# Optimization experiments

Measured on AMD Instinct MI355X. Metric: run time of the kernel, lower is better.

Reference implementation:

```python
import jax, jax.numpy as jnp
import numpy as np

N = 200000   # nodes
E = 600000   # directed edges
G = 8192     # graphs in batch
D_IN = 30
H = 128


def setup_inputs() -> dict:
    key = jax.random.key(0)
    ks = jax.random.split(key, 9)
    x = jax.random.normal(ks[0], (N, D_IN), jnp.float32)
    edge_index = jax.random.randint(ks[1], (2, E), 0, N, dtype=jnp.int32)
    batch_idx = jnp.sort(jax.random.randint(ks[2], (N,), 0, G, dtype=jnp.int32))
    W1 = jax.random.normal(ks[3], (D_IN, H), jnp.float32) / np.sqrt(D_IN)
    b1 = jnp.zeros((H,), jnp.float32)
    W2 = jax.random.normal(ks[4], (H, H), jnp.float32) / np.sqrt(H)
    b2 = jnp.zeros((H,), jnp.float32)
    W3 = jax.random.normal(ks[5], (H, H), jnp.float32) / np.sqrt(H)
    b3 = jnp.zeros((H,), jnp.float32)
    return {"x": x, "edge_index": edge_index, "batch_idx": batch_idx,
            "W1": W1, "b1": b1, "W2": W2, "b2": b2, "W3": W3, "b3": b3}


def _gcn_layer(x, W, b, src, dst, dinv):
    h = x @ W                                   # [N, H]
    norm = (dinv[src] * dinv[dst])[:, None]     # per-edge normalization
    msg = h[src] * norm                         # [E, H] gather + scale
    agg = jax.ops.segment_sum(msg, dst, num_segments=N)
    agg = agg + h * (dinv * dinv)[:, None]      # self-loop term, norm = 1/deg
    return jax.nn.relu(agg + b)


def reference(x, edge_index, batch_idx, W1, b1, W2, b2, W3, b3):
    src, dst = edge_index[0], edge_index[1]
    # degree with self-loops (edge weight 1), aggregated at target (col)
    deg = 1.0 + jax.ops.segment_sum(jnp.ones((E,), x.dtype), dst, num_segments=N)
    dinv = jax.lax.rsqrt(deg)                   # deg >= 1, safe
    h = _gcn_layer(x, W1, b1, src, dst, dinv)
    h = _gcn_layer(h, W2, b2, src, dst, dinv)
    h = _gcn_layer(h, W3, b3, src, dst, dinv)
    # global mean pool over batch segments
    sums = jax.ops.segment_sum(h, batch_idx, num_segments=G)
    counts = jax.ops.segment_sum(jnp.ones((N,), h.dtype), batch_idx, num_segments=G)
    return sums / jnp.maximum(counts, 1.0)[:, None]
```

## Files before the change

### kernel.cpp

```cpp
#include <hip/hip_runtime.h>


#define DIN 30
#define HD  128

typedef __attribute__((ext_vector_type(8))) short v8s;
typedef __attribute__((ext_vector_type(4))) float v4f;

static __device__ __forceinline__ unsigned short f2bf(float f) {
  unsigned int u = __float_as_uint(f);
  u += 0x7fffu + ((u >> 16) & 1u);
  return (unsigned short)(u >> 16);
}
static __device__ __forceinline__ float bf2f(unsigned short s) {
  return __uint_as_float(((unsigned int)s) << 16);
}
static __device__ __forceinline__ float bflo(unsigned int u) {
  return __uint_as_float(u << 16);
}
static __device__ __forceinline__ float bfhi(unsigned int u) {
  return __uint_as_float(u & 0xffff0000u);
}

__global__ void k_degree(const int* __restrict__ dst, int* __restrict__ deg,
                         int* __restrict__ eord, int E) {
  int e = blockIdx.x * blockDim.x + threadIdx.x;
  if (e < E) eord[e] = atomicAdd(&deg[dst[e]], 1);
}

__global__ void k_scan(const int* __restrict__ deg, int* __restrict__ scanbuf,
                       int* __restrict__ rowptr, float* __restrict__ dinv, int N) {
  __shared__ int s[256];
  __shared__ int sbase;
  int bid = blockIdx.x, tid = threadIdx.x;
  int base = bid * 1024 + tid * 4;
  int v[4]; int t = 0;
#pragma unroll
  for (int j = 0; j < 4; ++j) { int idx = base + j; v[j] = (idx < N) ? deg[idx] : 0; t += v[j]; }
  s[tid] = t; __syncthreads();
  for (int d = 1; d < 256; d <<= 1) {
    int u = (tid >= d) ? s[tid - d] : 0;
    __syncthreads();
    s[tid] += u;
    __syncthreads();
  }
  int myexcl = s[tid] - t;
  int blocktotal = s[255];
  if (tid == 0) atomicExch(&scanbuf[bid], blocktotal | 0x80000000);

  int pre = 0;
  for (int p = tid; p < bid; p += 256) {
    int val;
    do { val = atomicAdd(&scanbuf[p], 0); } while (!(val & 0x80000000));
    pre += val & 0x7fffffff;
  }
  __syncthreads();
  s[tid] = pre; __syncthreads();
  for (int d = 128; d > 0; d >>= 1) { if (tid < d) s[tid] += s[tid + d]; __syncthreads(); }
  if (tid == 0) sbase = s[0];
  __syncthreads();

  int run = sbase + myexcl;
#pragma unroll
  for (int j = 0; j < 4; ++j) {
    int idx = base + j;
    if (idx < N) {
      rowptr[idx] = run;
      dinv[idx] = rsqrtf((float)(1 + v[j]));
    }
    run += v[j];
    if (idx == N - 1) rowptr[N] = run;
  }
}

static __device__ __forceinline__ void wtf_one(const float* __restrict__ W,
                                               unsigned short* __restrict__ WTF,
                                               int idx, int Kreal, int KK) {
  int j = idx & 7;
  int c = idx >> 3;
  int l15 = c & 15;
  int quad = (c >> 4) & 3;
  int kk = (c >> 6) % KK;
  int t = c / (64 * KK);
  int k = kk * 32 + quad * 8 + j;
  int n = t * 16 + l15;
  WTF[idx] = (k < Kreal) ? f2bf(W[k * 128 + n]) : (unsigned short)0;
}

__global__ void k_prep(const int* __restrict__ src, const int* __restrict__ dst,
                       const int* __restrict__ rowptr, const int* __restrict__ eord,
                       int* __restrict__ col, int E,
                       const float* __restrict__ x, const float* __restrict__ dinv,
                       unsigned short* __restrict__ xb, int N,
                       const float* __restrict__ W1, const float* __restrict__ W2,
                       const float* __restrict__ W3,
                       unsigned short* __restrict__ W1F, unsigned short* __restrict__ W2F,
                       unsigned short* __restrict__ W3F,
                       const int* __restrict__ batch, int* __restrict__ gstart, int G,
                       float* __restrict__ out,
                       int SB, int XB, int WB, int BB) {
  int blk = blockIdx.x;
  if (blk < SB) {
    int e = blk * 256 + threadIdx.x;
    if (e < E) col[rowptr[dst[e]] + eord[e]] = src[e];
  } else if (blk < SB + XB) {
    int idx = (blk - SB) * 256 + threadIdx.x;
    if (idx < N * 32) {
      int n = idx >> 5, f = idx & 31;
      float v = (f < DIN) ? x[(size_t)n * DIN + f] * dinv[n] : 0.f;
      xb[idx] = f2bf(v);
    }
  } else if (blk < SB + XB + WB) {
    int idx = (blk - SB - XB) * 256 + threadIdx.x;
    if (idx < 4096) wtf_one(W1, W1F, idx, DIN, 1);
    else if (idx < 20480) wtf_one(W2, W2F, idx - 4096, 128, 4);
    else if (idx < 36864) wtf_one(W3, W3F, idx - 20480, 128, 4);
  } else if (blk < SB + XB + WB + BB) {
    int i = (blk - SB - XB - WB) * 256 + threadIdx.x;
    if (i >= N) return;
    int b = batch[i];
    int prev = (i == 0) ? -1 : batch[i - 1];
    for (int g = prev + 1; g <= b; ++g) gstart[g] = i;
    if (i == N - 1)
      for (int g = b + 1; g <= G; ++g) gstart[g] = N;
  } else {
    int idx = (blk - SB - XB - WB - BB) * 256 + threadIdx.x;
    if (idx < G * 32)
      ((float4*)out)[idx] = make_float4(0.f, 0.f, 0.f, 0.f);
  }
}

template <int K>
__global__ __launch_bounds__(1024, 8) void k_fused(const unsigned short* __restrict__ hin,
                                                   const unsigned short* __restrict__ WTF,
                                                   const float* __restrict__ b,
                                                   const int* __restrict__ rowptr,
                                                   const int* __restrict__ col,
                                                   const float* __restrict__ dinv,
                                                   unsigned short* __restrict__ C, int N) {
  constexpr int KK = K / 32;
  constexpr int KP = (K == 128) ? 136 : 40;
  constexpr int CP = 132;
  constexpr int SMSZ = (64 * KP > 64 * CP) ? 64 * KP : 64 * CP;
  __shared__ __align__(16) unsigned short sm[SMSZ];

  int tid = threadIdx.x;
  int l16 = tid & 15;
  int nl = tid >> 4;
  int row0 = blockIdx.x * 64;
  int node = row0 + nl;

  if (K == 32) {
    const unsigned int* hp = (const unsigned int*)hin;
    float a0 = 0.f, a1 = 0.f;
    if (node < N) {
      unsigned int u = hp[(size_t)node * 16 + l16];
      a0 = bflo(u); a1 = bfhi(u);
      int e0 = rowptr[node], e1 = rowptr[node + 1];
      int e = e0;
      for (; e + 2 <= e1; e += 2) {
        int c0 = col[e], c1 = col[e + 1];
        unsigned int v0 = hp[(size_t)c0 * 16 + l16];
        unsigned int v1 = hp[(size_t)c1 * 16 + l16];
        a0 += bflo(v0); a1 += bfhi(v0);
        a0 += bflo(v1); a1 += bfhi(v1);
      }
      if (e < e1) {
        unsigned int v0 = hp[(size_t)col[e] * 16 + l16];
        a0 += bflo(v0); a1 += bfhi(v0);
      }
      float di = dinv[node];
      a0 *= di; a1 *= di;
    }
    *(unsigned int*)&sm[nl * KP + l16 * 2] =
        (unsigned int)f2bf(a0) | ((unsigned int)f2bf(a1) << 16);
  } else {
    const uint4* hp = (const uint4*)hin;
    float a0 = 0.f, a1 = 0.f, a2 = 0.f, a3 = 0.f, a4 = 0.f, a5 = 0.f, a6 = 0.f, a7 = 0.f;
    if (node < N) {
      uint4 u = hp[(size_t)node * 16 + l16];
      a0 = bflo(u.x); a1 = bfhi(u.x);
      a2 = bflo(u.y); a3 = bfhi(u.y);
      a4 = bflo(u.z); a5 = bfhi(u.z);
      a6 = bflo(u.w); a7 = bfhi(u.w);
      int e0 = rowptr[node], e1 = rowptr[node + 1];
      int e = e0;
      for (; e + 2 <= e1; e += 2) {
        int c0 = col[e], c1 = col[e + 1];
        uint4 v0 = hp[(size_t)c0 * 16 + l16];
        uint4 v1 = hp[(size_t)c1 * 16 + l16];
        a0 += bflo(v0.x); a1 += bfhi(v0.x);
        a2 += bflo(v0.y); a3 += bfhi(v0.y);
        a4 += bflo(v0.z); a5 += bfhi(v0.z);
        a6 += bflo(v0.w); a7 += bfhi(v0.w);
        a0 += bflo(v1.x); a1 += bfhi(v1.x);
        a2 += bflo(v1.y); a3 += bfhi(v1.y);
        a4 += bflo(v1.z); a5 += bfhi(v1.z);
        a6 += bflo(v1.w); a7 += bfhi(v1.w);
      }
      if (e < e1) {
        uint4 v0 = hp[(size_t)col[e] * 16 + l16];
        a0 += bflo(v0.x); a1 += bfhi(v0.x);
        a2 += bflo(v0.y); a3 += bfhi(v0.y);
        a4 += bflo(v0.z); a5 += bfhi(v0.z);
        a6 += bflo(v0.w); a7 += bfhi(v0.w);
      }
      float di = dinv[node];
      a0 *= di; a1 *= di; a2 *= di; a3 *= di;
      a4 *= di; a5 *= di; a6 *= di; a7 *= di;
    }
    uint4 o;
    o.x = (unsigned int)f2bf(a0) | ((unsigned int)f2bf(a1) << 16);
    o.y = (unsigned int)f2bf(a2) | ((unsigned int)f2bf(a3) << 16);
    o.z = (unsigned int)f2bf(a4) | ((unsigned int)f2bf(a5) << 16);
    o.w = (unsigned int)f2bf(a6) | ((unsigned int)f2bf(a7) << 16);
    *(uint4*)&sm[nl * KP + l16 * 8] = o;
  }
  __syncthreads();

  int wv = tid >> 6, lane = tid & 63, quad = lane >> 4, l15 = lane & 15;
  int rt = wv & 3, tp = wv >> 2;
  v8s af[KK];
#pragma unroll
  for (int kk = 0; kk < KK; ++kk)
    af[kk] = *(const v8s*)&sm[(rt * 16 + l15) * KP + kk * 32 + quad * 8];
  __syncthreads();

  int crow0 = row0 + rt * 16 + quad * 4;
  float dr[4];
  if (crow0 + 3 < N) {
    float4 d4 = *(const float4*)&dinv[crow0];
    dr[0] = d4.x; dr[1] = d4.y; dr[2] = d4.z; dr[3] = d4.w;
  } else {
#pragma unroll
    for (int i = 0; i < 4; ++i) dr[i] = (crow0 + i < N) ? dinv[crow0 + i] : 0.f;
  }

#pragma unroll
  for (int tt = 0; tt < 2; ++tt) {
    int t = tp * 2 + tt;
    v4f acc = {0.f, 0.f, 0.f, 0.f};
#pragma unroll
    for (int kk = 0; kk < KK; ++kk) {
      v8s bf = *(const v8s*)(WTF + (size_t)(((t * KK + kk) * 4 + quad) * 16 + l15) * 8);
      acc = __builtin_amdgcn_mfma_f32_16x16x32_bf16(af[kk], bf, acc, 0, 0, 0);
    }
    float bias = b[t * 16 + l15];
#pragma unroll
    for (int i = 0; i < 4; ++i) {
      float o = fmaxf(acc[i] + bias, 0.f) * dr[i];
      sm[(rt * 16 + quad * 4 + i) * CP + t * 16 + l15] = f2bf(o);
    }
  }
  __syncthreads();

#pragma unroll
  for (int j = 0; j < 2; ++j) {
    int linear = j * 1024 + tid;
    int r = linear >> 5, ch = linear & 31;
    uint2 v = *(const uint2*)&sm[r * CP + ch * 4];
    int row = row0 + r;
    if (row < N) ((uint2*)C)[(size_t)row * 32 + ch] = v;
  }
}

__global__ __launch_bounds__(1024, 8) void k_fused_pool(const unsigned short* __restrict__ hin,
                                                        const unsigned short* __restrict__ WTF,
                                                        const float* __restrict__ b,
                                                        const int* __restrict__ rowptr,
                                                        const int* __restrict__ col,
                                                        const float* __restrict__ dinv,
                                                        const int* __restrict__ batch,
                                                        float* __restrict__ out, int N) {
  constexpr int KK = 4, KP = 136, CP = 132;
  constexpr int SMSZ = 64 * KP;
  __shared__ __align__(16) unsigned short sm[SMSZ];
  __shared__ int sbatch[64];

  int tid = threadIdx.x;
  int l16 = tid & 15;
  int nl = tid >> 4;
  int row0 = blockIdx.x * 64;
  int node = row0 + nl;

  if (tid < 64) sbatch[tid] = (row0 + tid < N) ? batch[row0 + tid] : -1;

  {
    const uint4* hp = (const uint4*)hin;
    float a0 = 0.f, a1 = 0.f, a2 = 0.f, a3 = 0.f, a4 = 0.f, a5 = 0.f, a6 = 0.f, a7 = 0.f;
    if (node < N) {
      uint4 u = hp[(size_t)node * 16 + l16];
      a0 = bflo(u.x); a1 = bfhi(u.x);
      a2 = bflo(u.y); a3 = bfhi(u.y);
      a4 = bflo(u.z); a5 = bfhi(u.z);
      a6 = bflo(u.w); a7 = bfhi(u.w);
      int e0 = rowptr[node], e1 = rowptr[node + 1];
      int e = e0;
      for (; e + 2 <= e1; e += 2) {
        int c0 = col[e], c1 = col[e + 1];
        uint4 v0 = hp[(size_t)c0 * 16 + l16];
        uint4 v1 = hp[(size_t)c1 * 16 + l16];
        a0 += bflo(v0.x); a1 += bfhi(v0.x);
        a2 += bflo(v0.y); a3 += bfhi(v0.y);
        a4 += bflo(v0.z); a5 += bfhi(v0.z);
        a6 += bflo(v0.w); a7 += bfhi(v0.w);
        a0 += bflo(v1.x); a1 += bfhi(v1.x);
        a2 += bflo(v1.y); a3 += bfhi(v1.y);
        a4 += bflo(v1.z); a5 += bfhi(v1.z);
        a6 += bflo(v1.w); a7 += bfhi(v1.w);
      }
      if (e < e1) {
        uint4 v0 = hp[(size_t)col[e] * 16 + l16];
        a0 += bflo(v0.x); a1 += bfhi(v0.x);
        a2 += bflo(v0.y); a3 += bfhi(v0.y);
        a4 += bflo(v0.z); a5 += bfhi(v0.z);
        a6 += bflo(v0.w); a7 += bfhi(v0.w);
      }
      float di = dinv[node];
      a0 *= di; a1 *= di; a2 *= di; a3 *= di;
      a4 *= di; a5 *= di; a6 *= di; a7 *= di;
    }
    uint4 o;
    o.x = (unsigned int)f2bf(a0) | ((unsigned int)f2bf(a1) << 16);
    o.y = (unsigned int)f2bf(a2) | ((unsigned int)f2bf(a3) << 16);
    o.z = (unsigned int)f2bf(a4) | ((unsigned int)f2bf(a5) << 16);
    o.w = (unsigned int)f2bf(a6) | ((unsigned int)f2bf(a7) << 16);
    *(uint4*)&sm[nl * KP + l16 * 8] = o;
  }
  __syncthreads();

  int wv = tid >> 6, lane = tid & 63, quad = lane >> 4, l15 = lane & 15;
  int rt = wv & 3, tp = wv >> 2;
  v8s af[KK];
#pragma unroll
  for (int kk = 0; kk < KK; ++kk)
    af[kk] = *(const v8s*)&sm[(rt * 16 + l15) * KP + kk * 32 + quad * 8];
  __syncthreads();

#pragma unroll
  for (int tt = 0; tt < 2; ++tt) {
    int t = tp * 2 + tt;
    v4f acc = {0.f, 0.f, 0.f, 0.f};
#pragma unroll
    for (int kk = 0; kk < KK; ++kk) {
      v8s bf = *(const v8s*)(WTF + (size_t)(((t * KK + kk) * 4 + quad) * 16 + l15) * 8);
      acc = __builtin_amdgcn_mfma_f32_16x16x32_bf16(af[kk], bf, acc, 0, 0, 0);
    }
    float bias = b[t * 16 + l15];
#pragma unroll
    for (int i = 0; i < 4; ++i) {
      float o = fmaxf(acc[i] + bias, 0.f);
      sm[(rt * 16 + quad * 4 + i) * CP + t * 16 + l15] = f2bf(o);
    }
  }
  __syncthreads();

  int f = tid & 127;
  int grp = tid >> 7;
  float run = 0.f;
  int cur = -1;
#pragma unroll
  for (int j = 0; j < 8; ++j) {
    int r = grp * 8 + j;
    int g = sbatch[r];
    if (g != cur) {
      if (cur >= 0) atomicAdd(&out[(size_t)cur * 128 + f], run);
      run = 0.f; cur = g;
    }
    if (g >= 0) run += bf2f(sm[r * CP + f]);
  }
  if (cur >= 0) atomicAdd(&out[(size_t)cur * 128 + f], run);
}

__global__ void k_finalize(float* __restrict__ out, const int* __restrict__ gstart, int G) {
  int idx = blockIdx.x * blockDim.x + threadIdx.x;
  if (idx >= G * 128) return;
  int g = idx >> 7;
  float cnt = (float)(gstart[g + 1] - gstart[g]);
  out[idx] = out[idx] / fmaxf(cnt, 1.f);
}

extern "C" void kernel_launch(void* const* d_in, const int* in_sizes, int n_in,
                              void* d_out, int out_size, void* d_ws, size_t ws_size,
                              hipStream_t stream) {
  const float* x  = (const float*)d_in[0];
  const int* ei   = (const int*)d_in[1];
  const int* batch = (const int*)d_in[2];
  const float* W1 = (const float*)d_in[3];
  const float* b1 = (const float*)d_in[4];
  const float* W2 = (const float*)d_in[5];
  const float* b2 = (const float*)d_in[6];
  const float* W3 = (const float*)d_in[7];
  const float* b3 = (const float*)d_in[8];
  float* out = (float*)d_out;
  int N = in_sizes[2];
  int E = in_sizes[1] / 2;
  int G = out_size / HD;
  const int* src = ei;
  const int* dst = ei + E;

  size_t off = 0;
  char* ws = (char*)d_ws;
  auto alloc = [&](size_t bytes) -> void* {
    void* p = ws + off;
    off += (bytes + 255) & ~(size_t)255;
    return p;
  };
  int nb1024 = (N + 1023) / 1024;
  int*   deg     = (int*)alloc((size_t)N * 4);
  int*   scanbuf = (int*)alloc((size_t)nb1024 * 4);
  float* dinv    = (float*)alloc((size_t)N * 4);
  int*   rowptr  = (int*)alloc((size_t)(N + 1) * 4);
  int*   eord    = (int*)alloc((size_t)E * 4);
  int*   col     = (int*)alloc((size_t)E * 4);
  int*   gstart  = (int*)alloc((size_t)(G + 1) * 4);
  unsigned short* xb  = (unsigned short*)alloc((size_t)N * 32 * 2);
  unsigned short* hA  = (unsigned short*)alloc((size_t)N * HD * 2);
  unsigned short* hB  = (unsigned short*)alloc((size_t)N * HD * 2);
  unsigned short* W1F = (unsigned short*)alloc(4096 * 2);
  unsigned short* W2F = (unsigned short*)alloc(16384 * 2);
  unsigned short* W3F = (unsigned short*)alloc(16384 * 2);
  (void)ws_size; (void)n_in;

  size_t zbytes = (size_t)((char*)dinv - (char*)deg);
  hipMemsetAsync(deg, 0, zbytes, stream);
  k_degree<<<(E + 255) / 256, 256, 0, stream>>>(dst, deg, eord, E);
  k_scan<<<nb1024, 256, 0, stream>>>(deg, scanbuf, rowptr, dinv, N);

  int SB = (E + 255) / 256;
  int XB = (N * 32 + 255) / 256;
  int WB = 144;
  int BB = (N + 255) / 256;
  int ZB = (G * 32 + 255) / 256;
  k_prep<<<SB + XB + WB + BB + ZB, 256, 0, stream>>>(src, dst, rowptr, eord, col, E,
                                                     x, dinv, xb, N,
                                                     W1, W2, W3, W1F, W2F, W3F,
                                                     batch, gstart, G, out,
                                                     SB, XB, WB, BB);

  int fusedBlocks = (N + 63) / 64;
  k_fused<32><<<fusedBlocks, 1024, 0, stream>>>(xb, W1F, b1, rowptr, col, dinv, hA, N);
  k_fused<128><<<fusedBlocks, 1024, 0, stream>>>(hA, W2F, b2, rowptr, col, dinv, hB, N);
  k_fused_pool<<<fusedBlocks, 1024, 0, stream>>>(hB, W3F, b3, rowptr, col, dinv, batch, out, N);
  k_finalize<<<(G * 128 + 255) / 256, 256, 0, stream>>>(out, gstart, G);
}
```

Measured before the change: 295.3 us.

## Sort CSR neighbor lists and sweep gathers in source-index windows for cache locality

Adds a kernel that insertion-sorts each node's neighbor column list, then restructures the gather loops in all three fused layers to walk source indices in windows, with a block-wide barrier between windows. All threads in a block then gather from the same region of the feature table at roughly the same time, which is meant to improve L2 hit rates on random gathers. In exchange it adds the sort kernel, roughly N/WDW barriers per block (about 13 for the 128-wide layers and 4 for the first layer), a dependent col load inside the loop, and loses the two-way unrolled loads.

```diff
diff --git a/kernel.cpp b/kernel.cpp
--- a/kernel.cpp
+++ b/kernel.cpp
@@ -130,6 +130,18 @@
   }
 }
 
+__global__ void k_sortrows(const int* __restrict__ rowptr, int* __restrict__ col, int N) {
+  int n = blockIdx.x * blockDim.x + threadIdx.x;
+  if (n >= N) return;
+  int e0 = rowptr[n], e1 = rowptr[n + 1];
+  for (int i = e0 + 1; i < e1; ++i) {
+    int v = col[i];
+    int j = i - 1;
+    while (j >= e0 && col[j] > v) { col[j + 1] = col[j]; --j; }
+    col[j + 1] = v;
+  }
+}
+
 template <int K>
 __global__ __launch_bounds__(1024, 8) void k_fused(const unsigned short* __restrict__ hin,
                                                    const unsigned short* __restrict__ WTF,
@@ -142,6 +154,7 @@
   constexpr int KP = (K == 128) ? 136 : 40;
   constexpr int CP = 132;
   constexpr int SMSZ = (64 * KP > 64 * CP) ? 64 * KP : 64 * CP;
+  constexpr int WDW = (K == 32) ? 65536 : 16384;
   __shared__ __align__(16) unsigned short sm[SMSZ];
 
   int tid = threadIdx.x;
@@ -153,22 +166,24 @@
   if (K == 32) {
     const unsigned int* hp = (const unsigned int*)hin;
     float a0 = 0.f, a1 = 0.f;
+    int e = 0, e1 = 0;
     if (node < N) {
       unsigned int u = hp[(size_t)node * 16 + l16];
       a0 = bflo(u); a1 = bfhi(u);
-      int e0 = rowptr[node], e1 = rowptr[node + 1];
-      int e = e0;
-      for (; e + 2 <= e1; e += 2) {
-        int c0 = col[e], c1 = col[e + 1];
-        unsigned int v0 = hp[(size_t)c0 * 16 + l16];
-        unsigned int v1 = hp[(size_t)c1 * 16 + l16];
-        a0 += bflo(v0); a1 += bfhi(v0);
-        a0 += bflo(v1); a1 += bfhi(v1);
-      }
-      if (e < e1) {
-        unsigned int v0 = hp[(size_t)col[e] * 16 + l16];
+      e = rowptr[node]; e1 = rowptr[node + 1];
+    }
+    int nc = (e < e1) ? col[e] : 0x7fffffff;
+    for (int lim = WDW;; lim += WDW) {
+      while (nc < lim) {
+        unsigned int v0 = hp[(size_t)nc * 16 + l16];
+        ++e;
+        nc = (e < e1) ? col[e] : 0x7fffffff;
         a0 += bflo(v0); a1 += bfhi(v0);
       }
+      if (lim >= N) break;
+      __syncthreads();
+    }
+    if (node < N) {
       float di = dinv[node];
       a0 *= di; a1 *= di;
     }
@@ -177,34 +192,30 @@
   } else {
     const uint4* hp = (const uint4*)hin;
     float a0 = 0.f, a1 = 0.f, a2 = 0.f, a3 = 0.f, a4 = 0.f, a5 = 0.f, a6 = 0.f, a7 = 0.f;
+    int e = 0, e1 = 0;
     if (node < N) {
       uint4 u = hp[(size_t)node * 16 + l16];
       a0 = bflo(u.x); a1 = bfhi(u.x);
       a2 = bflo(u.y); a3 = bfhi(u.y);
       a4 = bflo(u.z); a5 = bfhi(u.z);
       a6 = bflo(u.w); a7 = bfhi(u.w);
-      int e0 = rowptr[node], e1 = rowptr[node + 1];
-      int e = e0;
-      for (; e + 2 <= e1; e += 2) {
-        int c0 = col[e], c1 = col[e + 1];
-        uint4 v0 = hp[(size_t)c0 * 16 + l16];
-        uint4 v1 = hp[(size_t)c1 * 16 + l16];
-        a0 += bflo(v0.x); a1 += bfhi(v0.x);
-        a2 += bflo(v0.y); a3 += bfhi(v0.y);
-        a4 += bflo(v0.z); a5 += bfhi(v0.z);
-        a6 += bflo(v0.w); a7 += bfhi(v0.w);
-        a0 += bflo(v1.x); a1 += bfhi(v1.x);
-        a2 += bflo(v1.y); a3 += bfhi(v1.y);
-        a4 += bflo(v1.z); a5 += bfhi(v1.z);
-        a6 += bflo(v1.w); a7 += bfhi(v1.w);
-      }
-      if (e < e1) {
-        uint4 v0 = hp[(size_t)col[e] * 16 + l16];
+      e = rowptr[node]; e1 = rowptr[node + 1];
+    }
+    int nc = (e < e1) ? col[e] : 0x7fffffff;
+    for (int lim = WDW;; lim += WDW) {
+      while (nc < lim) {
+        uint4 v0 = hp[(size_t)nc * 16 + l16];
+        ++e;
+        nc = (e < e1) ? col[e] : 0x7fffffff;
         a0 += bflo(v0.x); a1 += bfhi(v0.x);
         a2 += bflo(v0.y); a3 += bfhi(v0.y);
         a4 += bflo(v0.z); a5 += bfhi(v0.z);
         a6 += bflo(v0.w); a7 += bfhi(v0.w);
       }
+      if (lim >= N) break;
+      __syncthreads();
+    }
+    if (node < N) {
       float di = dinv[node];
       a0 *= di; a1 *= di; a2 *= di; a3 *= di;
       a4 *= di; a5 *= di; a6 *= di; a7 *= di;
@@ -274,6 +285,7 @@
                                                         float* __restrict__ out, int N) {
   constexpr int KK = 4, KP = 136, CP = 132;
   constexpr int SMSZ = 64 * KP;
+  constexpr int WDW = 16384;
   __shared__ __align__(16) unsigned short sm[SMSZ];
   __shared__ int sbatch[64];
 
@@ -288,34 +300,30 @@
   {
     const uint4* hp = (const uint4*)hin;
     float a0 = 0.f, a1 = 0.f, a2 = 0.f, a3 = 0.f, a4 = 0.f, a5 = 0.f, a6 = 0.f, a7 = 0.f;
+    int e = 0, e1 = 0;
     if (node < N) {
       uint4 u = hp[(size_t)node * 16 + l16];
       a0 = bflo(u.x); a1 = bfhi(u.x);
       a2 = bflo(u.y); a3 = bfhi(u.y);
       a4 = bflo(u.z); a5 = bfhi(u.z);
       a6 = bflo(u.w); a7 = bfhi(u.w);
-      int e0 = rowptr[node], e1 = rowptr[node + 1];
-      int e = e0;
-      for (; e + 2 <= e1; e += 2) {
-        int c0 = col[e], c1 = col[e + 1];
-        uint4 v0 = hp[(size_t)c0 * 16 + l16];
-        uint4 v1 = hp[(size_t)c1 * 16 + l16];
-        a0 += bflo(v0.x); a1 += bfhi(v0.x);
-        a2 += bflo(v0.y); a3 += bfhi(v0.y);
-        a4 += bflo(v0.z); a5 += bfhi(v0.z);
-        a6 += bflo(v0.w); a7 += bfhi(v0.w);
-        a0 += bflo(v1.x); a1 += bfhi(v1.x);
-        a2 += bflo(v1.y); a3 += bfhi(v1.y);
-        a4 += bflo(v1.z); a5 += bfhi(v1.z);
-        a6 += bflo(v1.w); a7 += bfhi(v1.w);
-      }
-      if (e < e1) {
-        uint4 v0 = hp[(size_t)col[e] * 16 + l16];
+      e = rowptr[node]; e1 = rowptr[node + 1];
+    }
+    int nc = (e < e1) ? col[e] : 0x7fffffff;
+    for (int lim = WDW;; lim += WDW) {
+      while (nc < lim) {
+        uint4 v0 = hp[(size_t)nc * 16 + l16];
+        ++e;
+        nc = (e < e1) ? col[e] : 0x7fffffff;
         a0 += bflo(v0.x); a1 += bfhi(v0.x);
         a2 += bflo(v0.y); a3 += bfhi(v0.y);
         a4 += bflo(v0.z); a5 += bfhi(v0.z);
         a6 += bflo(v0.w); a7 += bfhi(v0.w);
       }
+      if (lim >= N) break;
+      __syncthreads();
+    }
+    if (node < N) {
       float di = dinv[node];
       a0 *= di; a1 *= di; a2 *= di; a3 *= di;
       a4 *= di; a5 *= di; a6 *= di; a7 *= di;
@@ -437,6 +445,7 @@
                                                      W1, W2, W3, W1F, W2F, W3F,
                                                      batch, gstart, G, out,
                                                      SB, XB, WB, BB);
+  k_sortrows<<<(N + 255) / 256, 256, 0, stream>>>(rowptr, col, N);
 
   int fusedBlocks = (N + 63) / 64;
   k_fused<32><<<fusedBlocks, 1024, 0, stream>>>(xb, W1F, b1, rowptr, col, dinv, hA, N);
```

Result: slower. 415.7 us (+40.8%).
